# Optimization experiments

Hardware: AMD Instinct MI355X
Metric: run time of the kernel (lower is better)

## Reference

```python
import jax, jax.numpy as jnp
import numpy as np

N = 204800   # total item nodes across the ragged batch
B = 4096     # number of session graphs
D = 256      # item_dim == output_dim
TAO = 1.0


def setup_inputs() -> dict:
    key = jax.random.key(0)
    k1, k2, k3, k4, k5, k6 = jax.random.split(key, 6)
    ifeat = jax.random.normal(k1, (N, D), dtype=jnp.float32)
    seg_ids = jnp.sort(jax.random.randint(k2, (N,), 0, B)).astype(jnp.int64)
    s = 1.0 / np.sqrt(D)
    Wu = jax.random.uniform(k3, (D, D), jnp.float32, -s, s)   # fc_u weight (no bias)
    Wv = jax.random.uniform(k4, (D, D), jnp.float32, -s, s)   # fc_v weight
    bv = jax.random.uniform(k5, (D,), jnp.float32, -s, s)     # fc_v bias
    we = jax.random.uniform(k6, (D,), jnp.float32, -s, s)     # fc_e weight -> scalar per node
    return {"ifeat": ifeat, "Wu": Wu, "Wv": Wv, "bv": bv, "we": we, "seg_ids": seg_ids}


def reference(ifeat, Wu, Wv, bv, we, seg_ids):
    seg = seg_ids.astype(jnp.int32)
    # anchor: segment mean of ifeat (pooling_type='imean')
    counts = jax.ops.segment_sum(jnp.ones((N,), ifeat.dtype), seg, num_segments=B)
    seg_sum = jax.ops.segment_sum(ifeat, seg, num_segments=B)          # [B, D]
    anchor = seg_sum / jnp.maximum(counts, 1.0)[:, None]               # [B, D]
    # attention logits
    ifeat_u = ifeat @ Wu.T                                             # [N, D]
    feat_v = (anchor @ Wv.T + bv)[seg]                                 # broadcast_nodes -> [N, D]
    e = jax.nn.sigmoid(ifeat_u + feat_v) @ we                          # [N]
    e = e / TAO
    # segment softmax over nodes of each session
    e_max = jax.ops.segment_max(e, seg, num_segments=B)                # [B]
    ex = jnp.exp(e - e_max[seg])                                       # [N]
    denom = jax.ops.segment_sum(ex, seg, num_segments=B)               # [B]
    alpha = ex / denom[seg]                                            # [N]
    # weighted segment sum
    rst = jax.ops.segment_sum(ifeat * alpha[:, None], seg, num_segments=B)  # [B, D]
    return jnp.concatenate([rst, anchor], axis=1)                      # [B, 2D]
```

## Files before the change

kernel.cpp:

```cpp
#include <hip/hip_runtime.h>
#include <hip/hip_bf16.h>

#define DD 256
#define NN 204800
#define SB 4096
#define ELEN 2048

typedef __attribute__((ext_vector_type(8))) short bf16x8;
typedef __attribute__((ext_vector_type(4))) float f32x4;

__device__ __forceinline__ unsigned short f2bf(float x) {
    union { float f; unsigned u; } v; v.f = x;
    unsigned r = v.u + 0x7FFF + ((v.u >> 16) & 1);
    return (unsigned short)(r >> 16);
}
__device__ __forceinline__ float bf2f(unsigned short h) {
    union { unsigned u; float f; } v; v.u = ((unsigned)h) << 16;
    return v.f;
}

__global__ void k_prep(const int* __restrict__ seg, const float* __restrict__ Wu,
                       int* __restrict__ seg_start, unsigned short* __restrict__ wub) {
    int blk = blockIdx.x, t = threadIdx.x;
    if (blk < 17) {
        int b = blk * 256 + t;
        if (b > SB) return;
        int lo = 0, hi = NN;
        while (lo < hi) {
            int mid = (lo + hi) >> 1;
            if (seg[mid] < b) lo = mid + 1; else hi = mid;
        }
        seg_start[b] = lo;
    } else {
        int o = (blk - 17) * 256 + t;
        int j    = o & 7;
        int colr = (o >> 3) & 15;
        int kg   = (o >> 7) & 3;
        int kt   = (o >> 9) & 7;
        int dt   = o >> 12;
        wub[o] = f2bf(Wu[(dt * 16 + colr) * DD + kt * 32 + kg * 8 + j]);
    }
}

__global__ __launch_bounds__(256) void k_anchor(
    const float* __restrict__ ifeat, const int* __restrict__ seg_start,
    unsigned short* __restrict__ xbf, float* __restrict__ anc_ws,
    float* __restrict__ out)
{
    __shared__ float ancp[4][DD];
    int b = blockIdx.x, t = threadIdx.x;
    int rg = t >> 6, ct = (t & 63) * 4;
    int s0 = seg_start[b], s1 = seg_start[b + 1];
    int C = s1 - s0;
    f32x4 asum = {0.f, 0.f, 0.f, 0.f};
    for (int i0 = 0; i0 < C; i0 += 4) {
        int i = i0 + rg;
        if (i < C) {
            const float4 v = *(const float4*)&ifeat[(size_t)(s0 + i) * DD + ct];
            asum.x += v.x; asum.y += v.y; asum.z += v.z; asum.w += v.w;
            ushort4 h;
            h.x = f2bf(v.x); h.y = f2bf(v.y); h.z = f2bf(v.z); h.w = f2bf(v.w);
            *(ushort4*)&xbf[(size_t)(s0 + i) * DD + ct] = h;
        }
    }
    *(f32x4*)&ancp[rg][ct] = asum;
    __syncthreads();
    float a = ancp[0][t] + ancp[1][t] + ancp[2][t] + ancp[3][t];
    float m = a / fmaxf((float)C, 1.f);
    anc_ws[b * DD + t] = m;
    out[(size_t)b * 2 * DD + DD + t] = m;
}

__global__ void k_featv(const float* __restrict__ anc_ws, const float* __restrict__ Wv,
                        const float* __restrict__ bv, float* __restrict__ feat_v) {
    int b0 = blockIdx.x * 16;
    int d = threadIdx.x;
    __shared__ float anc[16][DD];
    #pragma unroll
    for (int r = 0; r < 16; ++r) anc[r][d] = anc_ws[(b0 + r) * DD + d];
    __syncthreads();
    float acc[16];
    float bvd = bv[d];
    #pragma unroll
    for (int r = 0; r < 16; ++r) acc[r] = bvd;
    for (int k = 0; k < DD; k += 4) {
        float4 wv4 = *(const float4*)&Wv[d * DD + k];
        #pragma unroll
        for (int r = 0; r < 16; ++r) {
            acc[r] += wv4.x * anc[r][k] + wv4.y * anc[r][k + 1]
                    + wv4.z * anc[r][k + 2] + wv4.w * anc[r][k + 3];
        }
    }
    #pragma unroll
    for (int r = 0; r < 16; ++r) feat_v[(b0 + r) * DD + d] = acc[r];
}

__global__ __launch_bounds__(256, 3) void k_e(
    const unsigned short* __restrict__ xbf,
    const unsigned short* __restrict__ wub,
    const float* __restrict__ feat_v,
    const float* __restrict__ we,
    const int* __restrict__ seg,
    float* __restrict__ e_ws)
{
    const int t = threadIdx.x;
    const int w = t >> 6, lane = t & 63;
    const int colr = lane & 15, kg = lane >> 4;
    const int wbase = blockIdx.x * 128 + w * 32;

    bf16x8 a[2][8];
    {
        const unsigned short* ap = &xbf[(size_t)(wbase + colr) * DD + kg * 8];
        #pragma unroll
        for (int rt = 0; rt < 2; ++rt)
            #pragma unroll
            for (int kt = 0; kt < 8; ++kt)
                a[rt][kt] = *(const bf16x8*)(ap + rt * 16 * DD + kt * 32);
    }

    int sgv[2][4];
    #pragma unroll
    for (int rt = 0; rt < 2; ++rt)
        #pragma unroll
        for (int r = 0; r < 4; ++r)
            sgv[rt][r] = seg[wbase + rt * 16 + kg * 4 + r];

    float epart[2][4];
    #pragma unroll
    for (int rt = 0; rt < 2; ++rt)
        #pragma unroll
        for (int r = 0; r < 4; ++r) epart[rt][r] = 0.f;

    const unsigned short* bp = &wub[lane * 8];

    #pragma unroll 1
    for (int dt = 0; dt < 16; ++dt) {
        bf16x8 bfr[8];
        #pragma unroll
        for (int kt = 0; kt < 8; ++kt)
            bfr[kt] = *(const bf16x8*)(bp + (size_t)(dt * 8 + kt) * 512);

        f32x4 acc0 = (f32x4){0.f, 0.f, 0.f, 0.f};
        f32x4 acc1 = (f32x4){0.f, 0.f, 0.f, 0.f};
        #pragma unroll
        for (int kt = 0; kt < 8; ++kt) {
            acc0 = __builtin_amdgcn_mfma_f32_16x16x32_bf16(a[0][kt], bfr[kt], acc0, 0, 0, 0);
            acc1 = __builtin_amdgcn_mfma_f32_16x16x32_bf16(a[1][kt], bfr[kt], acc1, 0, 0, 0);
        }

        const float wed = we[dt * 16 + colr];
        #pragma unroll
        for (int r = 0; r < 4; ++r) {
            float fv0 = feat_v[(size_t)sgv[0][r] * DD + dt * 16 + colr];
            float fv1 = feat_v[(size_t)sgv[1][r] * DD + dt * 16 + colr];
            float u0 = acc0[r] + fv0;
            float u1 = acc1[r] + fv1;
            epart[0][r] += wed * __builtin_amdgcn_rcpf(1.f + __expf(-u0));
            epart[1][r] += wed * __builtin_amdgcn_rcpf(1.f + __expf(-u1));
        }
    }

    #pragma unroll
    for (int rt = 0; rt < 2; ++rt) {
        #pragma unroll
        for (int r = 0; r < 4; ++r) {
            float p = epart[rt][r];
            p += __shfl_xor(p, 1, 64);
            p += __shfl_xor(p, 2, 64);
            p += __shfl_xor(p, 4, 64);
            p += __shfl_xor(p, 8, 64);
            if (colr == 0) e_ws[wbase + rt * 16 + kg * 4 + r] = p;
        }
    }
}

__global__ __launch_bounds__(256) void k_rst(
    const unsigned short* __restrict__ xbf, const float* __restrict__ e_ws,
    const int* __restrict__ seg_start, float* __restrict__ out)
{
    int b = blockIdx.x, t = threadIdx.x;
    int s0 = seg_start[b], s1 = seg_start[b + 1];
    int C = s1 - s0;
    if (C <= 0) { out[(size_t)b * 2 * DD + t] = 0.f; return; }
    __shared__ float e_lds[ELEN];
    __shared__ float part[4][DD];
    __shared__ float red[4];
    __shared__ float bmx, bsum;
    int lane = t & 63, w = t >> 6;
    int Ce = (C < ELEN) ? C : ELEN;

    float m = -1e30f;
    for (int i = t; i < Ce; i += 256) m = fmaxf(m, e_ws[s0 + i]);
    #pragma unroll
    for (int off = 1; off < 64; off <<= 1) m = fmaxf(m, __shfl_xor(m, off, 64));
    if (lane == 0) red[w] = m;
    __syncthreads();
    if (t == 0) bmx = fmaxf(fmaxf(red[0], red[1]), fmaxf(red[2], red[3]));
    __syncthreads();
    m = bmx;
    float s = 0.f;
    for (int i = t; i < Ce; i += 256) {
        float ex = __expf(e_ws[s0 + i] - m);
        e_lds[i] = ex;
        s += ex;
    }
    #pragma unroll
    for (int off = 1; off < 64; off <<= 1) s += __shfl_xor(s, off, 64);
    if (lane == 0) red[w] = s;
    __syncthreads();
    if (t == 0) bsum = red[0] + red[1] + red[2] + red[3];
    __syncthreads();
    const float inv = 1.f / bsum;

    int rg = t >> 6, ct = (t & 63) * 4;
    f32x4 racc = {0.f, 0.f, 0.f, 0.f};
    for (int i0 = 0; i0 < C; i0 += 4) {
        int i = i0 + rg;
        if (i < C) {
            float al = (i < ELEN) ? e_lds[i] : 0.f;
            ushort4 v = *(const ushort4*)&xbf[(size_t)(s0 + i) * DD + ct];
            racc.x += al * bf2f(v.x);
            racc.y += al * bf2f(v.y);
            racc.z += al * bf2f(v.z);
            racc.w += al * bf2f(v.w);
        }
    }
    *(f32x4*)&part[rg][ct] = racc;
    __syncthreads();
    out[(size_t)b * 2 * DD + t] = (part[0][t] + part[1][t] + part[2][t] + part[3][t]) * inv;
}

extern "C" void kernel_launch(void* const* d_in, const int* in_sizes, int n_in,
                              void* d_out, int out_size, void* d_ws, size_t ws_size,
                              hipStream_t stream) {
    const float* ifeat = (const float*)d_in[0];
    const float* Wu    = (const float*)d_in[1];
    const float* Wv    = (const float*)d_in[2];
    const float* bv    = (const float*)d_in[3];
    const float* we    = (const float*)d_in[4];
    const int*   seg   = (const int*)d_in[5];
    float* out = (float*)d_out;

    char* ws = (char*)d_ws;
    int* seg_start        = (int*)ws;
    unsigned short* wub   = (unsigned short*)(ws + 32768);
    float* anc_ws         = (float*)(ws + 32768 + 131072);
    float* feat_v         = (float*)(ws + 32768 + 131072 + 4194304);
    float* e_ws           = (float*)(ws + 32768 + 131072 + 8388608);
    unsigned short* xbf   = (unsigned short*)(ws + 32768 + 131072 + 8388608 + 819200);

    k_prep<<<dim3(273), dim3(256), 0, stream>>>(seg, Wu, seg_start, wub);
    k_anchor<<<dim3(SB), dim3(256), 0, stream>>>(ifeat, seg_start, xbf, anc_ws, out);
    k_featv<<<dim3(SB / 16), dim3(256), 0, stream>>>(anc_ws, Wv, bv, feat_v);
    k_e<<<dim3(NN / 128), dim3(256), 0, stream>>>(xbf, wub, feat_v, we, seg, e_ws);
    k_rst<<<dim3(SB), dim3(256), 0, stream>>>(xbf, e_ws, seg_start, out);
}
```

Before: 184.1 us.

## Stage Wu tiles through double-buffered LDS and drop softmax max pass

In k_e, the bf16 Wu fragments now go into a double-buffered shared-memory tile: each block loads the next 4096-element slice while MFMAs consume the current one, instead of every wave fetching B fragments from global memory. k_e also writes exp(e) directly, so k_rst skips the segment-max pass and the LDS staging of exponentials and reads alpha numerators straight from e_ws. This cuts redundant global traffic and a reduction pass. In exchange it adds a block barrier per iteration, and dropping max subtraction relies on the logits being bounded, which holds because |e| <= sum|we| for sigmoid inputs.

After: 157.9 us. -14.3%, faster.

```diff
diff --git a/kernel.cpp b/kernel.cpp
--- a/kernel.cpp
+++ b/kernel.cpp
@@ -4,7 +4,6 @@
 #define DD 256
 #define NN 204800
 #define SB 4096
-#define ELEN 2048
 
 typedef __attribute__((ext_vector_type(8))) short bf16x8;
 typedef __attribute__((ext_vector_type(4))) float f32x4;
@@ -103,6 +102,7 @@
     const int* __restrict__ seg,
     float* __restrict__ e_ws)
 {
+    __shared__ unsigned short bsh[2][4096];
     const int t = threadIdx.x;
     const int w = t >> 6, lane = t & 63;
     const int colr = lane & 15, kg = lane >> 4;
@@ -131,21 +131,31 @@
         #pragma unroll
         for (int r = 0; r < 4; ++r) epart[rt][r] = 0.f;
 
-    const unsigned short* bp = &wub[lane * 8];
-
-    #pragma unroll 1
+    {
+        const uint4* s = (const uint4*)&wub[t * 16];
+        uint4 v0 = s[0], v1 = s[1];
+        *(uint4*)&bsh[0][t * 16] = v0;
+        *(uint4*)&bsh[0][t * 16 + 8] = v1;
+    }
+    __syncthreads();
+
+    #pragma unroll 2
     for (int dt = 0; dt < 16; ++dt) {
-        bf16x8 bfr[8];
-        #pragma unroll
-        for (int kt = 0; kt < 8; ++kt)
-            bfr[kt] = *(const bf16x8*)(bp + (size_t)(dt * 8 + kt) * 512);
+        const int cur = dt & 1;
+        if (dt < 15) {
+            const uint4* s = (const uint4*)&wub[(dt + 1) * 4096 + t * 16];
+            uint4 v0 = s[0], v1 = s[1];
+            *(uint4*)&bsh[cur ^ 1][t * 16] = v0;
+            *(uint4*)&bsh[cur ^ 1][t * 16 + 8] = v1;
+        }
 
         f32x4 acc0 = (f32x4){0.f, 0.f, 0.f, 0.f};
         f32x4 acc1 = (f32x4){0.f, 0.f, 0.f, 0.f};
         #pragma unroll
         for (int kt = 0; kt < 8; ++kt) {
-            acc0 = __builtin_amdgcn_mfma_f32_16x16x32_bf16(a[0][kt], bfr[kt], acc0, 0, 0, 0);
-            acc1 = __builtin_amdgcn_mfma_f32_16x16x32_bf16(a[1][kt], bfr[kt], acc1, 0, 0, 0);
+            bf16x8 bfr = *(const bf16x8*)&bsh[cur][kt * 512 + lane * 8];
+            acc0 = __builtin_amdgcn_mfma_f32_16x16x32_bf16(a[0][kt], bfr, acc0, 0, 0, 0);
+            acc1 = __builtin_amdgcn_mfma_f32_16x16x32_bf16(a[1][kt], bfr, acc1, 0, 0, 0);
         }
 
         const float wed = we[dt * 16 + colr];
@@ -158,6 +168,7 @@
             epart[0][r] += wed * __builtin_amdgcn_rcpf(1.f + __expf(-u0));
             epart[1][r] += wed * __builtin_amdgcn_rcpf(1.f + __expf(-u1));
         }
+        __syncthreads();
     }
 
     #pragma unroll
@@ -169,7 +180,7 @@
             p += __shfl_xor(p, 2, 64);
             p += __shfl_xor(p, 4, 64);
             p += __shfl_xor(p, 8, 64);
-            if (colr == 0) e_ws[wbase + rt * 16 + kg * 4 + r] = p;
+            if (colr == 0) e_ws[wbase + rt * 16 + kg * 4 + r] = __expf(p);
         }
     }
 }
@@ -182,28 +193,13 @@
     int s0 = seg_start[b], s1 = seg_start[b + 1];
     int C = s1 - s0;
     if (C <= 0) { out[(size_t)b * 2 * DD + t] = 0.f; return; }
-    __shared__ float e_lds[ELEN];
     __shared__ float part[4][DD];
     __shared__ float red[4];
-    __shared__ float bmx, bsum;
+    __shared__ float bsum;
     int lane = t & 63, w = t >> 6;
-    int Ce = (C < ELEN) ? C : ELEN;
-
-    float m = -1e30f;
-    for (int i = t; i < Ce; i += 256) m = fmaxf(m, e_ws[s0 + i]);
-    #pragma unroll
-    for (int off = 1; off < 64; off <<= 1) m = fmaxf(m, __shfl_xor(m, off, 64));
-    if (lane == 0) red[w] = m;
-    __syncthreads();
-    if (t == 0) bmx = fmaxf(fmaxf(red[0], red[1]), fmaxf(red[2], red[3]));
-    __syncthreads();
-    m = bmx;
+
     float s = 0.f;
-    for (int i = t; i < Ce; i += 256) {
-        float ex = __expf(e_ws[s0 + i] - m);
-        e_lds[i] = ex;
-        s += ex;
-    }
+    for (int i = t; i < C; i += 256) s += e_ws[s0 + i];
     #pragma unroll
     for (int off = 1; off < 64; off <<= 1) s += __shfl_xor(s, off, 64);
     if (lane == 0) red[w] = s;
@@ -217,7 +213,7 @@
     for (int i0 = 0; i0 < C; i0 += 4) {
         int i = i0 + rg;
         if (i < C) {
-            float al = (i < ELEN) ? e_lds[i] : 0.f;
+            float al = e_ws[s0 + i];
             ushort4 v = *(const ushort4*)&xbf[(size_t)(s0 + i) * DD + ct];
             racc.x += al * bf2f(v.x);
             racc.y += al * bf2f(v.y);
```
